# Kernel optimization log

Hardware: AMD Instinct MI355X
Metric: run time of the kernel (lower is better)

## Reference

```python
import jax, jax.numpy as jnp
import numpy as np

GROUPS = 8          # 4-bit groups per row (one scale/offset each)
VALS_PER_GROUP = 8  # nibbles packed per int32 weight word
MID = GROUPS * VALS_PER_GROUP  # fixed inner dim = 64


def _unpack4(x, n):
    """Unpack n little-endian 4-bit nibbles from int32 array x -> [..., n]."""
    shifts = (jnp.arange(n, dtype=jnp.int32) * 4)
    return jnp.right_shift(x[..., None], shifts) & 15


def setup_inputs() -> dict:
    key = jax.random.key(0)
    k1, k2, k3, k4 = jax.random.split(key, 4)
    N0, N1 = 8192, 8192
    scale = jax.random.normal(k1, (N0, GROUPS), dtype=jnp.float32)
    offset = jax.random.randint(k2, (N0,), 0, 2147483647, dtype=jnp.int32)
    weight = jax.random.randint(k3, (N0, GROUPS), 0, 2147483647, dtype=jnp.int32)
    activation = jax.random.normal(k4, (MID, N1), dtype=jnp.float32)
    return {"scale": scale, "offset": offset, "weight": weight, "activation": activation}


def reference(scale, offset, weight, activation):
    # weight: [N0, 8] int32, each word packs 8 nibbles -> [N0, 8, 8] -> MID=64
    w = _unpack4(weight, VALS_PER_GROUP).astype(jnp.float32)   # [N0, G, V]
    # offset: [N0] int32 packs one 4-bit offset per group -> [N0, G]
    off = _unpack4(offset, GROUPS).astype(jnp.float32)         # [N0, G]
    # per-group dequant: scale * (w - offset)
    dq = scale[:, :, None] * (w - off[:, :, None])             # [N0, G, V]
    dq = dq.reshape(scale.shape[0], MID)                       # [N0, 64]
    return dq @ activation                                     # [N0, N1]
```

## Files before the change

kernel.cpp:

```cpp
#include <hip/hip_runtime.h>
#include <hip/hip_bf16.h>

#define M_DIM 8192
#define N_DIM 8192

typedef short short8 __attribute__((ext_vector_type(8)));
typedef float f32x4 __attribute__((ext_vector_type(4)));

static __device__ __forceinline__ short f2bf(float f) {
    __hip_bfloat16 h = __float2bfloat16(f);
    union { __hip_bfloat16 h; short s; } u;
    u.h = h;
    return u.s;
}

__global__ __launch_bounds__(256, 2) void gemm_dq(const float* __restrict__ scale,
                                                  const int* __restrict__ offset,
                                                  const int* __restrict__ weight,
                                                  const float* __restrict__ act,
                                                  float* __restrict__ C) {
    __shared__ float cs[4][16 * 132];

    const int tid  = threadIdx.x;
    const int lane = tid & 63;
    const int wid  = tid >> 6;
    const int l15  = lane & 15;
    const int l4   = lane >> 4;

    const int bn = (int)blockIdx.x & 63;
    const int mg = (int)blockIdx.x >> 6;
    const int n0 = bn * 128;

    short8 bfrag[2][8];
    #pragma unroll
    for (int kh = 0; kh < 2; ++kh) {
        #pragma unroll
        for (int fn = 0; fn < 8; ++fn) {
            const float* ap = act + (size_t)(kh * 32 + l4 * 8) * N_DIM + (n0 + fn * 16 + l15);
            short8 b;
            #pragma unroll
            for (int j = 0; j < 8; ++j) {
                b[j] = f2bf(ap[(size_t)j * N_DIM]);
            }
            bfrag[kh][fn] = b;
        }
    }

    float* ws = &cs[wid][0];
    const int rot = ((mg >> 2) & 1) * 4;

    #pragma unroll 2
    for (int ti = 0; ti < 8; ++ti) {
        const int t  = (ti + rot) & 7;
        const int m0 = (mg * 8 + t) * 128 + wid * 32;

        #pragma unroll
        for (int fm = 0; fm < 2; ++fm) {
            short8 afrag[2];
            #pragma unroll
            for (int kh = 0; kh < 2; ++kh) {
                const int g = kh * 4 + l4;
                const int m = m0 + fm * 16 + l15;
                const unsigned w = (unsigned)weight[m * 8 + g];
                const float   s = scale[m * 8 + g];
                const int   off = (int)(((unsigned)offset[m] >> (4 * g)) & 15u);
                short8 a;
                #pragma unroll
                for (int j = 0; j < 8; ++j) {
                    const int wv = (int)((w >> (4 * j)) & 15u);
                    a[j] = f2bf(s * (float)(wv - off));
                }
                afrag[kh] = a;
            }

            f32x4 acc[8] = {};
            #pragma unroll
            for (int fn = 0; fn < 8; ++fn) {
                acc[fn] = __builtin_amdgcn_mfma_f32_16x16x32_bf16(
                    afrag[0], bfrag[0][fn], acc[fn], 0, 0, 0);
                acc[fn] = __builtin_amdgcn_mfma_f32_16x16x32_bf16(
                    afrag[1], bfrag[1][fn], acc[fn], 0, 0, 0);
            }

            #pragma unroll
            for (int fn = 0; fn < 8; ++fn) {
                const int col = fn * 16 + l15;
                #pragma unroll
                for (int j = 0; j < 4; ++j) {
                    const int row16 = l4 * 4 + j;
                    ws[row16 * 132 + col] = acc[fn][j];
                }
            }
            asm volatile("s_waitcnt lgkmcnt(0)" ::: "memory");

            #pragma unroll
            for (int s = 0; s < 8; ++s) {
                const int row16 = s * 2 + (lane >> 5);
                const int c4    = (lane & 31) * 4;
                const f32x4 v = *reinterpret_cast<const f32x4*>(&ws[row16 * 132 + c4]);
                const size_t gr = (size_t)(m0 + fm * 16 + row16);
                __builtin_nontemporal_store(v, reinterpret_cast<f32x4*>(
                    &C[gr * N_DIM + n0 + c4]));
            }
        }
    }
}

extern "C" void kernel_launch(void* const* d_in, const int* in_sizes, int n_in,
                              void* d_out, int out_size, void* d_ws, size_t ws_size,
                              hipStream_t stream) {
    const float* scale  = (const float*)d_in[0];
    const int*   offset = (const int*)d_in[1];
    const int*   weight = (const int*)d_in[2];
    const float* act    = (const float*)d_in[3];
    float* out  = (float*)d_out;

    gemm_dq<<<512, 256, 0, stream>>>(scale, offset, weight, act, out);
}
```

Before: 51.15 us.

## Widen block N tile to 256 columns and halve M iterations per block

Each block now covers 256 output columns instead of 128, holding 16 bf16 activation fragments per wave in registers, and makes 4 M-tile passes instead of 8. Each converted activation fragment is now reused across more columns of work per block, and each output row is written as one 1 KB contiguous line per wave. The cost is doubled register pressure from the larger bfrag array, larger LDS staging, and the removal of the unroll-2 pragma. That may reduce occupancy or cause spills under launch_bounds(256,2).

Measured after the change: 76.16 us. 48.9% more time.

```diff
diff --git a/kernel.cpp b/kernel.cpp
--- a/kernel.cpp
+++ b/kernel.cpp
@@ -19,7 +19,7 @@
                                                   const int* __restrict__ weight,
                                                   const float* __restrict__ act,
                                                   float* __restrict__ C) {
-    __shared__ float cs[4][16 * 132];
+    __shared__ float cs[4][16 * 260];
 
     const int tid  = threadIdx.x;
     const int lane = tid & 63;
@@ -27,15 +27,15 @@
     const int l15  = lane & 15;
     const int l4   = lane >> 4;
 
-    const int bn = (int)blockIdx.x & 63;
-    const int mg = (int)blockIdx.x >> 6;
-    const int n0 = bn * 128;
+    const int bn = (int)blockIdx.x & 31;
+    const int mg = (int)blockIdx.x >> 5;
+    const int n0 = bn * 256;
 
-    short8 bfrag[2][8];
+    short8 bfrag[2][16];
     #pragma unroll
     for (int kh = 0; kh < 2; ++kh) {
         #pragma unroll
-        for (int fn = 0; fn < 8; ++fn) {
+        for (int fn = 0; fn < 16; ++fn) {
             const float* ap = act + (size_t)(kh * 32 + l4 * 8) * N_DIM + (n0 + fn * 16 + l15);
             short8 b;
             #pragma unroll
@@ -47,12 +47,11 @@
     }
 
     float* ws = &cs[wid][0];
-    const int rot = ((mg >> 2) & 1) * 4;
+    const int rot = ((mg >> 3) & 1) * 2;
 
-    #pragma unroll 2
-    for (int ti = 0; ti < 8; ++ti) {
-        const int t  = (ti + rot) & 7;
-        const int m0 = (mg * 8 + t) * 128 + wid * 32;
+    for (int ti = 0; ti < 4; ++ti) {
+        const int t  = (ti + rot) & 3;
+        const int m0 = mg * 512 + t * 128 + wid * 32;
 
         #pragma unroll
         for (int fm = 0; fm < 2; ++fm) {
@@ -73,34 +72,35 @@
                 afrag[kh] = a;
             }
 
-            f32x4 acc[8] = {};
             #pragma unroll
-            for (int fn = 0; fn < 8; ++fn) {
-                acc[fn] = __builtin_amdgcn_mfma_f32_16x16x32_bf16(
-                    afrag[0], bfrag[0][fn], acc[fn], 0, 0, 0);
-                acc[fn] = __builtin_amdgcn_mfma_f32_16x16x32_bf16(
-                    afrag[1], bfrag[1][fn], acc[fn], 0, 0, 0);
-            }
-
-            #pragma unroll
-            for (int fn = 0; fn < 8; ++fn) {
-                const int col = fn * 16 + l15;
+            for (int h = 0; h < 2; ++h) {
+                f32x4 acc[8] = {};
                 #pragma unroll
-                for (int j = 0; j < 4; ++j) {
-                    const int row16 = l4 * 4 + j;
-                    ws[row16 * 132 + col] = acc[fn][j];
+                for (int f = 0; f < 8; ++f) {
+                    const int fn = h * 8 + f;
+                    acc[f] = __builtin_amdgcn_mfma_f32_16x16x32_bf16(
+                        afrag[0], bfrag[0][fn], acc[f], 0, 0, 0);
+                    acc[f] = __builtin_amdgcn_mfma_f32_16x16x32_bf16(
+                        afrag[1], bfrag[1][fn], acc[f], 0, 0, 0);
+                }
+                #pragma unroll
+                for (int f = 0; f < 8; ++f) {
+                    const int col = (h * 8 + f) * 16 + l15;
+                    #pragma unroll
+                    for (int j = 0; j < 4; ++j) {
+                        const int row16 = l4 * 4 + j;
+                        ws[row16 * 260 + col] = acc[f][j];
+                    }
                 }
             }
             asm volatile("s_waitcnt lgkmcnt(0)" ::: "memory");
 
             #pragma unroll
-            for (int s = 0; s < 8; ++s) {
-                const int row16 = s * 2 + (lane >> 5);
-                const int c4    = (lane & 31) * 4;
-                const f32x4 v = *reinterpret_cast<const f32x4*>(&ws[row16 * 132 + c4]);
-                const size_t gr = (size_t)(m0 + fm * 16 + row16);
+            for (int r = 0; r < 16; ++r) {
+                const f32x4 v = *reinterpret_cast<const f32x4*>(&ws[r * 260 + lane * 4]);
+                const size_t gr = (size_t)(m0 + fm * 16 + r);
                 __builtin_nontemporal_store(v, reinterpret_cast<f32x4*>(
-                    &C[gr * N_DIM + n0 + c4]));
+                    &C[gr * N_DIM + n0 + lane * 4]));
             }
         }
     }
```
